# Performance work log

Measured on AMD Instinct MI355X. Metric: run time of the kernel, lower is better.

The kernel has to match this reference:

```python
import jax, jax.numpy as jnp
import numpy as np

N_NODES = 100000
N_EDGES = 1000000
N_GRAPHS = 4096
F_IN = 9
H = 64


def setup_inputs() -> dict:
    key = jax.random.key(0)
    ks = jax.random.split(key, 12)
    x = jax.random.normal(ks[0], (N_NODES, F_IN), dtype=jnp.float32)
    edge_index = jax.random.randint(ks[1], (2, N_EDGES), 0, N_NODES, dtype=jnp.int64)
    batch = jnp.sort(jax.random.randint(ks[2], (N_NODES,), 0, N_GRAPHS, dtype=jnp.int64))
    def lin(k, fan_in, fan_out):
        s = 1.0 / np.sqrt(fan_in)
        return jax.random.uniform(k, (fan_in, fan_out), jnp.float32, -s, s)
    return {
        "x": x, "edge_index": edge_index, "batch": batch,
        "W1": lin(ks[3], F_IN, H), "b1": jnp.zeros((H,), jnp.float32),
        "W2": lin(ks[4], H, H),    "b2": jnp.zeros((H,), jnp.float32),
        "W3": lin(ks[5], H, H),    "b3": jnp.zeros((H,), jnp.float32),
        "W4": lin(ks[6], H, H),    "b4": jnp.zeros((H,), jnp.float32),
        "Wout": lin(ks[7], H, 1),  "bout": jnp.zeros((1,), jnp.float32),
    }


def reference(x, edge_index, batch, W1, b1, W2, b2, W3, b3, W4, b4, Wout, bout):
    N = x.shape[0]
    loops = jnp.arange(N, dtype=edge_index.dtype)
    src = jnp.concatenate([edge_index[0], loops])  # messages flow src -> dst (PyG source_to_target)
    dst = jnp.concatenate([edge_index[1], loops])
    # symmetric GCN normalization with self-loops: deg includes self-loop
    deg = jax.ops.segment_sum(jnp.ones_like(dst, dtype=x.dtype), dst, num_segments=N)
    dis = jax.lax.rsqrt(jnp.maximum(deg, 1.0))  # deg >= 1 thanks to self-loops
    norm = dis[src] * dis[dst]                  # [E+N]

    def gcn_conv(h, W, b):
        h = h @ W                                # transform first (PyG order)
        msgs = h[src] * norm[:, None]            # [E+N, H]
        return jax.ops.segment_sum(msgs, dst, num_segments=N) + b

    h = jax.nn.relu(gcn_conv(x, W1, b1))
    h = jax.nn.relu(gcn_conv(h, W2, b2))
    h = jax.nn.relu(gcn_conv(h, W3, b3))
    h = jax.nn.relu(gcn_conv(h, W4, b4))

    # global mean pool over graphs
    sums = jax.ops.segment_sum(h, batch, num_segments=N_GRAPHS)      # [G, H]
    counts = jax.ops.segment_sum(jnp.ones((N,), h.dtype), batch, num_segments=N_GRAPHS)
    pooled = sums / jnp.maximum(counts, 1.0)[:, None]
    return pooled @ Wout + bout                  # [G, 1]
```

## Files before the change

### kernel.cpp

```cpp
#include <hip/hip_runtime.h>
#include <hip/hip_fp16.h>


static inline size_t align256(size_t x){ return (x + 255) & ~size_t(255); }

#define CHUNK 4096
#define SCAP  3072

struct __align__(8)  h4v { __half2 a, b; };
struct __align__(16) h8v { __half2 a, b, c, d; };

typedef _Float16 f16x8 __attribute__((ext_vector_type(8)));
typedef float    f32x4 __attribute__((ext_vector_type(4)));

__global__ __launch_bounds__(256) void k_sortchunk(
    const int* __restrict__ src, const int* __restrict__ dst,
    int* __restrict__ binned, int* __restrict__ hoffC, int E){
  __shared__ int hcnt[1024];
  __shared__ int simg[CHUNK];
  int c = blockIdx.x, t = threadIdx.x;
  int e0 = c*CHUNK;
  int cnt = E - e0; if (cnt > CHUNK) cnt = CHUNK;

  for (int i = t; i < 1024; i += 256) hcnt[i] = 0;
  __syncthreads();

  int bA[8], rA[8], vA[8], bB[8], rB[8], vB[8];
  #pragma unroll
  for (int j = 0; j < 8; j++){
    int i = t + j*256;
    if (i < cnt){
      int d = dst[e0+i];
      int s = src[e0+i];
      int b = d >> 7;
      bA[j] = b;
      rA[j] = atomicAdd(&hcnt[b], 1);
      vA[j] = (s << 7) | (d & 127);
    } else bA[j] = -1;
  }
  #pragma unroll
  for (int j = 0; j < 8; j++){
    int i = t + 2048 + j*256;
    if (i < cnt){
      int d = dst[e0+i];
      int s = src[e0+i];
      int b = d >> 7;
      bB[j] = b;
      rB[j] = atomicAdd(&hcnt[b], 1);
      vB[j] = (s << 7) | (d & 127);
    } else bB[j] = -1;
  }
  __syncthreads();

  int own[4];
  #pragma unroll
  for (int j = 0; j < 4; j++) own[j] = hcnt[t + j*256];
  for (int off = 1; off < 1024; off <<= 1){
    int nv[4];
    #pragma unroll
    for (int j = 0; j < 4; j++){
      int i = t + j*256;
      nv[j] = hcnt[i] + ((i >= off) ? hcnt[i-off] : 0);
    }
    __syncthreads();
    #pragma unroll
    for (int j = 0; j < 4; j++) hcnt[t + j*256] = nv[j];
    __syncthreads();
  }
  #pragma unroll
  for (int j = 0; j < 4; j++) hcnt[t + j*256] -= own[j];
  __syncthreads();

  for (int i = t; i < 783; i += 256) hoffC[c*783 + i] = hcnt[i];

  #pragma unroll
  for (int j = 0; j < 8; j++)
    if (bA[j] >= 0) simg[hcnt[bA[j]] + rA[j]] = vA[j];
  #pragma unroll
  for (int j = 0; j < 8; j++)
    if (bB[j] >= 0) simg[hcnt[bB[j]] + rB[j]] = vB[j];
  __syncthreads();

  for (int i = t; i < cnt; i += 256) binned[e0 + i] = simg[i];
}

__global__ __launch_bounds__(256) void k_bktsum(
    const int* __restrict__ hoffC, int* __restrict__ btot,
    float* __restrict__ gsum, int NC, int NBK, int G){
  __shared__ int s[256];
  int b = blockIdx.x, t = threadIdx.x;
  int gid = b*256 + t;
  if (gid < G) gsum[gid] = 0.f;
  int tot = 0;
  for (int c = t; c < NC; c += 256)
    tot += hoffC[c*783 + b + 1] - hoffC[c*783 + b];
  s[t] = tot; __syncthreads();
  for (int off = 128; off > 0; off >>= 1){
    if (t < off) s[t] += s[t+off];
    __syncthreads();
  }
  if (t == 0) btot[b] = s[0];
}

__global__ __launch_bounds__(256) void k_gather2(
    const int* __restrict__ binned, const int* __restrict__ hoffC,
    const int* __restrict__ btot, const float* __restrict__ x,
    int* __restrict__ row_ptr, float* __restrict__ dis,
    float* __restrict__ xs, int* __restrict__ csr, int N, int NC, int E){
  __shared__ int lcur[128];
  __shared__ int lscan[128];
  __shared__ float ldis[128];
  __shared__ int stage[SCAP];
  __shared__ int scount;
  __shared__ int sbb;
  int b = blockIdx.x, t = threadIdx.x;
  int n0 = b << 7;
  int nn = N - n0; if (nn > 128) nn = 128;

  int psum = 0;
  for (int i = t; i < b; i += 256) psum += btot[i];
  stage[t] = psum; __syncthreads();
  for (int off = 128; off > 0; off >>= 1){
    if (t < off) stage[t] += stage[t+off];
    __syncthreads();
  }
  if (t == 0) sbb = stage[0];
  if (t == 0 && b == 0) row_ptr[N] = E;
  if (t < 128) lcur[t] = 0;
  if (t == 0) scount = 0;
  __syncthreads();

  for (int c = t; c < NC; c += 256){
    int o0 = hoffC[c*783 + b];
    int o1 = hoffC[c*783 + b + 1];
    int len = o1 - o0;
    if (len > 0){
      int base = atomicAdd(&scount, len);
      int sbase = c*CHUNK;
      for (int k = 0; k < len; k++){
        int v = binned[sbase + o0 + k];
        atomicAdd(&lcur[v & 127], 1);
        int pos = base + k;
        if (pos < SCAP) stage[pos] = v;
      }
    }
  }
  __syncthreads();
  int degv = (t < 128) ? lcur[t] : 0;
  if (t < 128) lscan[t] = degv;
  __syncthreads();
  for (int off = 1; off < 128; off <<= 1){
    int add = (t < 128 && t >= off) ? lscan[t-off] : 0;
    __syncthreads();
    if (t < 128) lscan[t] += add;
    __syncthreads();
  }
  int bb = sbb;
  if (t < nn){
    int row = bb + lscan[t] - degv;
    row_ptr[n0 + t] = row;
    float dv = rsqrtf((float)(degv + 1));
    dis[n0 + t] = dv;
    ldis[t] = dv;
    lcur[t] = row;
  }
  __syncthreads();
  for (int i = t; i < nn*9; i += 256)
    xs[(size_t)n0*9 + i] = x[(size_t)n0*9 + i] * ldis[i/9];
  int sc = scount;
  if (sc <= SCAP){
    for (int i = t; i < sc; i += 256){
      int v = stage[i];
      int pos = atomicAdd(&lcur[v & 127], 1);
      csr[pos] = v >> 7;
    }
  } else {
    for (int c = t; c < NC; c += 256){
      int o0 = hoffC[c*783 + b];
      int o1 = hoffC[c*783 + b + 1];
      int sbase = c*CHUNK;
      for (int k = o0; k < o1; k++){
        int v = binned[sbase + k];
        int pos = atomicAdd(&lcur[v & 127], 1);
        csr[pos] = v >> 7;
      }
    }
  }
}

__global__ void k_agg9(const float* __restrict__ xs, const float* __restrict__ dis,
                       const int* __restrict__ row_ptr, const int* __restrict__ csr,
                       float* __restrict__ xagg, int N){
  int tid = blockIdx.x*blockDim.x + threadIdx.x;
  if (tid >= N*9) return;
  int n = tid/9, f = tid - n*9;
  float dn = dis[n];
  int s0 = row_ptr[n], s1 = row_ptr[n+1];
  float a0 = xs[tid];
  float a1 = 0.f, a2 = 0.f, a3 = 0.f;
  int j = s0;
  for (; j + 3 < s1; j += 4){
    int e0 = csr[j], e1 = csr[j+1], e2 = csr[j+2], e3 = csr[j+3];
    a0 += xs[e0*9+f];
    a1 += xs[e1*9+f];
    a2 += xs[e2*9+f];
    a3 += xs[e3*9+f];
  }
  for (; j < s1; j++) a0 += xs[csr[j]*9+f];
  xagg[tid] = ((a0+a1)+(a2+a3))*dn;
}

__device__ __forceinline__ void mfma_epilogue(
    const _Float16* hlw, const f16x8 (&wf)[4][2],
    __half* __restrict__ mo, int wid, int nwaves, int N, int lane){
  int lm = lane & 15, lk = lane >> 4;
  f16x8 hb0 = *(const f16x8*)(hlw + lm*72 + lk*8);
  f16x8 hb1 = *(const f16x8*)(hlw + lm*72 + 32 + lk*8);
  int node = wid + lm*nwaves;
  bool ok = (node < N);
  __half* row = mo + (size_t)node*64;
  #pragma unroll
  for (int ft = 0; ft < 4; ft++){
    f32x4 acc = {0.f, 0.f, 0.f, 0.f};
    acc = __builtin_amdgcn_mfma_f32_16x16x32_f16(wf[ft][0], hb0, acc, 0, 0, 0);
    acc = __builtin_amdgcn_mfma_f32_16x16x32_f16(wf[ft][1], hb1, acc, 0, 0, 0);
    if (ok){
      h4v o;
      o.a = __floats2half2_rn(acc[0], acc[1]);
      o.b = __floats2half2_rn(acc[2], acc[3]);
      *(h4v*)(row + ft*16 + lk*4) = o;
    }
  }
}

#define LOAD_WFRAGS(Wn)                                                    \
  f16x8 wf[4][2];                                                          \
  { int lm_ = lane & 15, lk_ = lane >> 4;                                  \
    _Pragma("unroll") for (int ft = 0; ft < 4; ft++)                       \
    _Pragma("unroll") for (int kb = 0; kb < 2; kb++)                       \
    _Pragma("unroll") for (int j = 0; j < 8; j++)                          \
      wf[ft][kb][j] = (_Float16)Wn[(kb*32 + lk_*8 + j)*64 + ft*16 + lm_]; }

__global__ __launch_bounds__(256) void k_lin1_fused(
    const float* __restrict__ xagg, const float* __restrict__ W1,
    const float* __restrict__ b1, const float* __restrict__ dis,
    const float* __restrict__ W2, __half* __restrict__ mo, int N, int nwaves){
  __shared__ float W1l[576];
  __shared__ float b1l[64];
  __shared__ _Float16 hl[4][16*72];
  int t = threadIdx.x;
  for (int i = t; i < 576; i += 256) W1l[i] = W1[i];
  if (t < 64) b1l[t] = b1[t];
  __syncthreads();
  int lane = t & 63, w = t >> 6;
  int wid = (blockIdx.x*blockDim.x + t) >> 6;
  LOAD_WFRAGS(W2)
  _Float16* hlw = hl[w];
  for (int i = 0; i < 16; i++){
    int n = wid + i*nwaves;
    _Float16 hv = (_Float16)0.f;
    if (n < N){
      float acc = b1l[lane];
      #pragma unroll
      for (int k = 0; k < 9; k++) acc = fmaf(xagg[n*9+k], W1l[k*64+lane], acc);
      hv = (_Float16)(fmaxf(acc, 0.f) * dis[n]);
    }
    hlw[i*72 + lane] = hv;
  }
  mfma_epilogue(hlw, wf, mo, wid, nwaves, N, lane);
}

#define ACC8(g_)  do{ float2 t_;                                   \
  t_ = __half22float2((g_).a); acc0 += t_.x; acc1 += t_.y;         \
  t_ = __half22float2((g_).b); acc2 += t_.x; acc3 += t_.y;         \
  t_ = __half22float2((g_).c); acc4 += t_.x; acc5 += t_.y;         \
  t_ = __half22float2((g_).d); acc6 += t_.x; acc7 += t_.y; }while(0)

#define RED3(v)  do{ v += __shfl_xor(v, 8,64);                     \
                     v += __shfl_xor(v,16,64);                     \
                     v += __shfl_xor(v,32,64); }while(0)

#define AGG_ISSUE(n_, rp0_, rp1_, rn0_, rn1_, e0_, e1_, g0_, g1_, sf_, dn_) \
  do{                                                                      \
    int nn_ = (n_) + 2*nwaves;                                             \
    rn0_ = 0; rn1_ = 0;                                                    \
    if (nn_ < N){ rn0_ = row_ptr[nn_]; rn1_ = row_ptr[nn_+1]; }            \
    e0_ = -1; e1_ = -1;                                                    \
    if ((n_) < N){                                                         \
      sf_ = m[(size_t)(n_)*8 + q2];                                        \
      dn_ = dis[n_];                                                       \
      int j0_ = (rp0_) + sub, j1_ = (rp0_) + 8 + sub;                      \
      if (j0_ < (rp1_)) e0_ = csr[j0_];                                    \
      if (j1_ < (rp1_)) e1_ = csr[j1_];                                    \
      if (e0_ >= 0) g0_ = m[(size_t)e0_*8 + q2];                           \
      if (e1_ >= 0) g1_ = m[(size_t)e1_*8 + q2];                           \
    }                                                                      \
  }while(0)

#define AGG_ACCRED(n_, rp0_, rp1_, e0_, e1_, g0_, g1_, sf_, dn_)           \
      float acc0=0.f,acc1=0.f,acc2=0.f,acc3=0.f;                           \
      float acc4=0.f,acc5=0.f,acc6=0.f,acc7=0.f;                           \
      if (e0_ >= 0) ACC8(g0_);                                             \
      if (e1_ >= 0) ACC8(g1_);                                             \
      for (int j_ = (rp0_) + 16 + sub; j_ < (rp1_); j_ += 8){              \
        h8v gx_ = m[(size_t)csr[j_]*8 + q2]; ACC8(gx_);                    \
      }                                                                    \
      RED3(acc0); RED3(acc1); RED3(acc2); RED3(acc3);                      \
      RED3(acc4); RED3(acc5); RED3(acc6); RED3(acc7);                      \
      float2 s01=__half22float2((sf_).a), s23=__half22float2((sf_).b);     \
      float2 s45=__half22float2((sf_).c), s67=__half22float2((sf_).d);     \
      float r0 = fmaxf(fmaf(acc0 + s01.x, dn_, bb0.x), 0.f);               \
      float r1 = fmaxf(fmaf(acc1 + s01.y, dn_, bb0.y), 0.f);               \
      float r2 = fmaxf(fmaf(acc2 + s23.x, dn_, bb0.z), 0.f);               \
      float r3 = fmaxf(fmaf(acc3 + s23.y, dn_, bb0.w), 0.f);               \
      float r4 = fmaxf(fmaf(acc4 + s45.x, dn_, bb1.x), 0.f);               \
      float r5 = fmaxf(fmaf(acc5 + s45.y, dn_, bb1.y), 0.f);               \
      float r6 = fmaxf(fmaf(acc6 + s67.x, dn_, bb1.z), 0.f);               \
      float r7 = fmaxf(fmaf(acc7 + s67.y, dn_, bb1.w), 0.f);

#define AGG_REDUCE(n_, rp0_, rp1_, e0_, e1_, g0_, g1_, sf_, dn_, i_)       \
  do{                                                                      \
    if ((n_) < N){                                                         \
      AGG_ACCRED(n_, rp0_, rp1_, e0_, e1_, g0_, g1_, sf_, dn_)             \
      if (sub == 0){                                                       \
        h8v hv_;                                                           \
        hv_.a = __floats2half2_rn(r0*(dn_), r1*(dn_));                     \
        hv_.b = __floats2half2_rn(r2*(dn_), r3*(dn_));                     \
        hv_.c = __floats2half2_rn(r4*(dn_), r5*(dn_));                     \
        hv_.d = __floats2half2_rn(r6*(dn_), r7*(dn_));                     \
        *(h8v*)(hlw + (i_)*72 + q2*8) = hv_;                               \
      }                                                                    \
    } else if (sub == 0){                                                  \
      h8v z_; z_.a = __floats2half2_rn(0.f, 0.f);                          \
      z_.b = z_.a; z_.c = z_.a; z_.d = z_.a;                               \
      *(h8v*)(hlw + (i_)*72 + q2*8) = z_;                                  \
    }                                                                      \
  }while(0)

__global__ __launch_bounds__(256) void k_agg_fused(
    const h8v* __restrict__ m, const float* __restrict__ dis,
    const float* __restrict__ b, const float* __restrict__ Wn,
    const int* __restrict__ row_ptr, const int* __restrict__ csr,
    __half* __restrict__ mo, int N, int nwaves){
  __shared__ _Float16 hl[4][16*72];
  int t = threadIdx.x;
  int lane = t & 63, w = t >> 6;
  int sub = lane >> 3, q2 = lane & 7;
  int wid = (blockIdx.x*blockDim.x + t) >> 6;
  _Float16* hlw = hl[w];
  const float4* b4 = (const float4*)b;
  float4 bb0 = b4[q2*2], bb1 = b4[q2*2+1];

  int nA = wid,          rA0 = 0, rA1 = 0;
  int nB = wid + nwaves, rB0 = 0, rB1 = 0;
  if (nA < N){ rA0 = row_ptr[nA]; rA1 = row_ptr[nA+1]; }
  if (nB < N){ rB0 = row_ptr[nB]; rB1 = row_ptr[nB+1]; }
  int eA0, eA1, eB0, eB1, rnA0, rnA1, rnB0, rnB1;
  h8v gA0, gA1, sfA, gB0, gB1, sfB;
  float dnA = 0.f, dnB = 0.f;
  AGG_ISSUE(nA, rA0, rA1, rnA0, rnA1, eA0, eA1, gA0, gA1, sfA, dnA);
  for (int p = 0; p < 8; p++){
    AGG_ISSUE(nB, rB0, rB1, rnB0, rnB1, eB0, eB1, gB0, gB1, sfB, dnB);
    AGG_REDUCE(nA, rA0, rA1, eA0, eA1, gA0, gA1, sfA, dnA, 2*p);
    nA += 2*nwaves; rA0 = rnA0; rA1 = rnA1;
    if (p < 7)
      AGG_ISSUE(nA, rA0, rA1, rnA0, rnA1, eA0, eA1, gA0, gA1, sfA, dnA);
    AGG_REDUCE(nB, rB0, rB1, eB0, eB1, gB0, gB1, sfB, dnB, 2*p+1);
    nB += 2*nwaves; rB0 = rnB0; rB1 = rnB1;
  }
  LOAD_WFRAGS(Wn)
  mfma_epilogue(hlw, wf, mo, wid, nwaves, N, lane);
}

__global__ __launch_bounds__(256) void k_agg64_out(
    const h8v* __restrict__ m, const float* __restrict__ dis,
    const float* __restrict__ b, const float* __restrict__ Wout,
    const int* __restrict__ batch,
    const int* __restrict__ row_ptr, const int* __restrict__ csr,
    float* gsum, int N, int nwaves){
  int lane = threadIdx.x & 63;
  int sub = lane >> 3, q2 = lane & 7;
  int n = (blockIdx.x*blockDim.x + threadIdx.x) >> 6;
  if (n >= N) return;
  const float4* b4 = (const float4*)b;
  const float4* wo4 = (const float4*)Wout;
  float4 bb0 = b4[q2*2], bb1 = b4[q2*2+1];
  float4 w0 = wo4[q2*2], w1 = wo4[q2*2+1];

  int rp0 = row_ptr[n], rp1 = row_ptr[n+1];
  int n1 = n + nwaves;
  int rq0 = 0, rq1 = 0;
  if (n1 < N){ rq0 = row_ptr[n1]; rq1 = row_ptr[n1+1]; }
  int e0 = -1, e1 = -1;
  { int j0 = rp0 + sub, j1 = rp0 + 8 + sub;
    if (j0 < rp1) e0 = csr[j0];
    if (j1 < rp1) e1 = csr[j1]; }
  while (true){
    h8v g0, g1, sf;
    if (e0 >= 0) g0 = m[(size_t)e0*8 + q2];
    if (e1 >= 0) g1 = m[(size_t)e1*8 + q2];
    sf = m[(size_t)n*8 + q2];
    float dn = dis[n];
    int bg = batch[n];
    int n2 = n1 + nwaves;
    int rr0 = 0, rr1 = 0;
    if (n2 < N){ rr0 = row_ptr[n2]; rr1 = row_ptr[n2+1]; }
    int f0 = -1, f1 = -1;
    if (n1 < N){
      int j0 = rq0 + sub, j1 = rq0 + 8 + sub;
      if (j0 < rq1) f0 = csr[j0];
      if (j1 < rq1) f1 = csr[j1];
    }
    AGG_ACCRED(n, rp0, rp1, e0, e1, g0, g1, sf, dn)
    float p = r0*w0.x + r1*w0.y + r2*w0.z + r3*w0.w
            + r4*w1.x + r5*w1.y + r6*w1.z + r7*w1.w;
    p += __shfl_xor(p,1,64); p += __shfl_xor(p,2,64); p += __shfl_xor(p,4,64);
    if (lane == 0) atomicAdd(&gsum[bg], p);
    if (n1 >= N) break;
    n = n1; rp0 = rq0; rp1 = rq1;
    n1 = n2; rq0 = rr0; rq1 = rr1;
    e0 = f0; e1 = f1;
  }
}

__global__ void k_final(const float* __restrict__ gsum, const int* __restrict__ batch,
                        const float* __restrict__ bout, float* __restrict__ out,
                        int G, int N){
  int g = blockIdx.x*blockDim.x + threadIdx.x;
  if (g >= G) return;
  int lo = 0, hi = N;
  while (lo < hi){ int mid = (lo+hi)>>1; if (batch[mid] <  g) lo = mid+1; else hi = mid; }
  int lb = lo;
  lo = 0; hi = N;
  while (lo < hi){ int mid = (lo+hi)>>1; if (batch[mid] <= g) lo = mid+1; else hi = mid; }
  int c = lo - lb;
  out[g] = gsum[g]/(float)(c > 0 ? c : 1) + bout[0];
}

extern "C" void kernel_launch(void* const* d_in, const int* in_sizes, int n_in,
                              void* d_out, int out_size, void* d_ws, size_t ws_size,
                              hipStream_t stream){
  const float* x    = (const float*)d_in[0];
  const int*   ei   = (const int*)d_in[1];
  const int*   batch= (const int*)d_in[2];
  const float* W1 = (const float*)d_in[3];  const float* b1 = (const float*)d_in[4];
  const float* W2 = (const float*)d_in[5];  const float* b2 = (const float*)d_in[6];
  const float* W3 = (const float*)d_in[7];  const float* b3 = (const float*)d_in[8];
  const float* W4 = (const float*)d_in[9];  const float* b4 = (const float*)d_in[10];
  const float* Wout = (const float*)d_in[11]; const float* bout = (const float*)d_in[12];
  float* out = (float*)d_out;

  const int N = in_sizes[0]/9;
  const int E = in_sizes[1]/2;
  const int G = out_size;
  const int* src = ei;
  const int* dst = ei + E;

  char* ws = (char*)d_ws;
  size_t off = 0;
  auto alloc = [&](size_t bytes){ void* p = ws + off; off = align256(off + bytes); return p; };
  int*   row_ptr  = (int*)  alloc((size_t)(N+1)*4);
  int*   csr      = (int*)  alloc((size_t)E*4);
  float* dis      = (float*)alloc((size_t)N*4);
  const int NBK = (N + 127)/128;
  const int NC  = (E + CHUNK-1)/CHUNK;
  int*   hoffC    = (int*)  alloc((size_t)NC*783*4);
  int*   btot     = (int*)  alloc((size_t)NBK*4);
  float* gsum     = (float*)alloc((size_t)G*4);
  __half* mA      = (__half*)alloc((size_t)N*64*2);
  __half* mB      = (__half*)alloc((size_t)N*64*2);
  int*   binned   = (int*)mA;
  float* xs       = (float*)mB;
  float* xagg     = xs + (size_t)N*9;

  const int AGG_BLOCKS = 2048;
  const int AGG_WAVES  = AGG_BLOCKS*4;

  k_sortchunk<<<NC, 256, 0, stream>>>(src, dst, binned, hoffC, E);
  k_bktsum   <<<NBK, 256, 0, stream>>>(hoffC, btot, gsum, NC, NBK, G);
  k_gather2  <<<NBK, 256, 0, stream>>>(binned, hoffC, btot, x,
                                       row_ptr, dis, xs, csr, N, NC, E);

  k_agg9  <<<(N*9+255)/256, 256, 0, stream>>>(xs, dis, row_ptr, csr, xagg, N);
  k_lin1_fused<<<AGG_BLOCKS, 256, 0, stream>>>(xagg, W1, b1, dis, W2, mA, N, AGG_WAVES);

  k_agg_fused<<<AGG_BLOCKS, 256, 0, stream>>>((const h8v*)mA, dis, b2, W3,
                                              row_ptr, csr, mB, N, AGG_WAVES);
  k_agg_fused<<<AGG_BLOCKS, 256, 0, stream>>>((const h8v*)mB, dis, b3, W4,
                                              row_ptr, csr, mA, N, AGG_WAVES);
  k_agg64_out<<<AGG_BLOCKS, 256, 0, stream>>>((const h8v*)mA, dis, b4, Wout, batch,
                                              row_ptr, csr, gsum, N, AGG_WAVES);

  k_final<<<(G+255)/256, 256, 0, stream>>>(gsum, batch, bout, out, G, N);
}
```

Measured before the change: 299.7 us.

## Pad input features to 12 floats and aggregate layer-1 per node with float4

Scaled input features are stored padded to 12 floats per node so the first aggregation can run one thread per node with three float4 gathers per neighbor, instead of nine scalar threads per node each re-reading the CSR indices. The final aggregation kernel also drops its cross-iteration software pipelining of row pointers and neighbor indices in favor of a simpler loop that loads edges and features inline. The padding adds 33% more storage and traffic for xs and xagg, and the one-thread-per-node layout gives less parallelism and uncoalesced per-thread loads.

```diff
diff --git a/kernel.cpp b/kernel.cpp
--- a/kernel.cpp
+++ b/kernel.cpp
@@ -165,8 +165,11 @@
     lcur[t] = row;
   }
   __syncthreads();
-  for (int i = t; i < nn*9; i += 256)
-    xs[(size_t)n0*9 + i] = x[(size_t)n0*9 + i] * ldis[i/9];
+  for (int i = t; i < nn*12; i += 256){
+    int node = i/12, f = i - node*12;
+    xs[(size_t)(n0+node)*12 + f] =
+        (f < 9) ? x[(size_t)(n0+node)*9 + f] * ldis[node] : 0.f;
+  }
   int sc = scount;
   if (sc <= SCAP){
     for (int i = t; i < sc; i += 256){
@@ -188,26 +191,38 @@
   }
 }
 
-__global__ void k_agg9(const float* __restrict__ xs, const float* __restrict__ dis,
-                       const int* __restrict__ row_ptr, const int* __restrict__ csr,
-                       float* __restrict__ xagg, int N){
-  int tid = blockIdx.x*blockDim.x + threadIdx.x;
-  if (tid >= N*9) return;
-  int n = tid/9, f = tid - n*9;
+#define F4ADD(d_, s_) do{ d_.x += s_.x; d_.y += s_.y; d_.z += s_.z; d_.w += s_.w; }while(0)
+
+__global__ __launch_bounds__(256) void k_agg9(
+    const float4* __restrict__ xs4, const float* __restrict__ dis,
+    const int* __restrict__ row_ptr, const int* __restrict__ csr,
+    float4* __restrict__ xagg4, int N){
+  int n = blockIdx.x*blockDim.x + threadIdx.x;
+  if (n >= N) return;
   float dn = dis[n];
   int s0 = row_ptr[n], s1 = row_ptr[n+1];
-  float a0 = xs[tid];
-  float a1 = 0.f, a2 = 0.f, a3 = 0.f;
+  float4 a0 = xs4[(size_t)n*3], a1 = xs4[(size_t)n*3+1], a2 = xs4[(size_t)n*3+2];
+  float4 b0 = {0,0,0,0}, b1 = b0, b2 = b0;
   int j = s0;
-  for (; j + 3 < s1; j += 4){
-    int e0 = csr[j], e1 = csr[j+1], e2 = csr[j+2], e3 = csr[j+3];
-    a0 += xs[e0*9+f];
-    a1 += xs[e1*9+f];
-    a2 += xs[e2*9+f];
-    a3 += xs[e3*9+f];
-  }
-  for (; j < s1; j++) a0 += xs[csr[j]*9+f];
-  xagg[tid] = ((a0+a1)+(a2+a3))*dn;
+  for (; j + 1 < s1; j += 2){
+    int e0 = csr[j], e1 = csr[j+1];
+    float4 p0 = xs4[(size_t)e0*3], p1 = xs4[(size_t)e0*3+1], p2 = xs4[(size_t)e0*3+2];
+    float4 q0 = xs4[(size_t)e1*3], q1 = xs4[(size_t)e1*3+1], q2 = xs4[(size_t)e1*3+2];
+    F4ADD(a0,p0); F4ADD(a1,p1); F4ADD(a2,p2);
+    F4ADD(b0,q0); F4ADD(b1,q1); F4ADD(b2,q2);
+  }
+  if (j < s1){
+    int e0 = csr[j];
+    float4 p0 = xs4[(size_t)e0*3], p1 = xs4[(size_t)e0*3+1], p2 = xs4[(size_t)e0*3+2];
+    F4ADD(a0,p0); F4ADD(a1,p1); F4ADD(a2,p2);
+  }
+  F4ADD(a0,b0); F4ADD(a1,b1); F4ADD(a2,b2);
+  a0.x *= dn; a0.y *= dn; a0.z *= dn; a0.w *= dn;
+  a1.x *= dn; a1.y *= dn; a1.z *= dn; a1.w *= dn;
+  a2.x *= dn; a2.y *= dn; a2.z *= dn; a2.w *= dn;
+  xagg4[(size_t)n*3]   = a0;
+  xagg4[(size_t)n*3+1] = a1;
+  xagg4[(size_t)n*3+2] = a2;
 }
 
 __device__ __forceinline__ void mfma_epilogue(
@@ -262,7 +277,7 @@
     if (n < N){
       float acc = b1l[lane];
       #pragma unroll
-      for (int k = 0; k < 9; k++) acc = fmaf(xagg[n*9+k], W1l[k*64+lane], acc);
+      for (int k = 0; k < 9; k++) acc = fmaf(xagg[(size_t)n*12+k], W1l[k*64+lane], acc);
       hv = (_Float16)(fmaxf(acc, 0.f) * dis[n]);
     }
     hlw[i*72 + lane] = hv;
@@ -382,44 +397,44 @@
   int sub = lane >> 3, q2 = lane & 7;
   int n = (blockIdx.x*blockDim.x + threadIdx.x) >> 6;
   if (n >= N) return;
+  int rp0 = row_ptr[n], rp1 = row_ptr[n+1];
   const float4* b4 = (const float4*)b;
   const float4* wo4 = (const float4*)Wout;
-  float4 bb0 = b4[q2*2], bb1 = b4[q2*2+1];
-  float4 w0 = wo4[q2*2], w1 = wo4[q2*2+1];
-
-  int rp0 = row_ptr[n], rp1 = row_ptr[n+1];
-  int n1 = n + nwaves;
-  int rq0 = 0, rq1 = 0;
-  if (n1 < N){ rq0 = row_ptr[n1]; rq1 = row_ptr[n1+1]; }
-  int e0 = -1, e1 = -1;
-  { int j0 = rp0 + sub, j1 = rp0 + 8 + sub;
-    if (j0 < rp1) e0 = csr[j0];
-    if (j1 < rp1) e1 = csr[j1]; }
   while (true){
-    h8v g0, g1, sf;
-    if (e0 >= 0) g0 = m[(size_t)e0*8 + q2];
-    if (e1 >= 0) g1 = m[(size_t)e1*8 + q2];
-    sf = m[(size_t)n*8 + q2];
+    int nn = n + nwaves;
+    int np0 = 0, np1 = 0;
+    if (nn < N){ np0 = row_ptr[nn]; np1 = row_ptr[nn+1]; }
+    h8v sf = m[(size_t)n*8 + q2];
     float dn = dis[n];
     int bg = batch[n];
-    int n2 = n1 + nwaves;
-    int rr0 = 0, rr1 = 0;
-    if (n2 < N){ rr0 = row_ptr[n2]; rr1 = row_ptr[n2+1]; }
-    int f0 = -1, f1 = -1;
-    if (n1 < N){
-      int j0 = rq0 + sub, j1 = rq0 + 8 + sub;
-      if (j0 < rq1) f0 = csr[j0];
-      if (j1 < rq1) f1 = csr[j1];
-    }
-    AGG_ACCRED(n, rp0, rp1, e0, e1, g0, g1, sf, dn)
+    float acc0=0.f,acc1=0.f,acc2=0.f,acc3=0.f,acc4=0.f,acc5=0.f,acc6=0.f,acc7=0.f;
+    int s1 = rp1;
+    int j0 = rp0 + sub, j1 = rp0 + 8 + sub;
+    if (j0 < s1){ h8v a = m[(size_t)csr[j0]*8 + q2]; ACC8(a); }
+    if (j1 < s1){ h8v a = m[(size_t)csr[j1]*8 + q2]; ACC8(a); }
+    for (int j = rp0 + 16 + sub; j < s1; j += 8){
+      h8v a = m[(size_t)csr[j]*8 + q2]; ACC8(a);
+    }
+    RED3(acc0); RED3(acc1); RED3(acc2); RED3(acc3);
+    RED3(acc4); RED3(acc5); RED3(acc6); RED3(acc7);
+    float2 s01 = __half22float2(sf.a), s23 = __half22float2(sf.b);
+    float2 s45 = __half22float2(sf.c), s67 = __half22float2(sf.d);
+    float4 bb0 = b4[q2*2], bb1 = b4[q2*2+1];
+    float4 w0 = wo4[q2*2], w1 = wo4[q2*2+1];
+    float r0 = fmaxf(fmaf(acc0 + s01.x, dn, bb0.x), 0.f);
+    float r1 = fmaxf(fmaf(acc1 + s01.y, dn, bb0.y), 0.f);
+    float r2 = fmaxf(fmaf(acc2 + s23.x, dn, bb0.z), 0.f);
+    float r3 = fmaxf(fmaf(acc3 + s23.y, dn, bb0.w), 0.f);
+    float r4 = fmaxf(fmaf(acc4 + s45.x, dn, bb1.x), 0.f);
+    float r5 = fmaxf(fmaf(acc5 + s45.y, dn, bb1.y), 0.f);
+    float r6 = fmaxf(fmaf(acc6 + s67.x, dn, bb1.z), 0.f);
+    float r7 = fmaxf(fmaf(acc7 + s67.y, dn, bb1.w), 0.f);
     float p = r0*w0.x + r1*w0.y + r2*w0.z + r3*w0.w
             + r4*w1.x + r5*w1.y + r6*w1.z + r7*w1.w;
     p += __shfl_xor(p,1,64); p += __shfl_xor(p,2,64); p += __shfl_xor(p,4,64);
     if (lane == 0) atomicAdd(&gsum[bg], p);
-    if (n1 >= N) break;
-    n = n1; rp0 = rq0; rp1 = rq1;
-    n1 = n2; rq0 = rr0; rq1 = rr1;
-    e0 = f0; e1 = f1;
+    if (nn >= N) break;
+    n = nn; rp0 = np0; rp1 = np1;
   }
 }
 
@@ -471,7 +486,7 @@
   __half* mB      = (__half*)alloc((size_t)N*64*2);
   int*   binned   = (int*)mA;
   float* xs       = (float*)mB;
-  float* xagg     = xs + (size_t)N*9;
+  float* xagg     = xs + (size_t)N*12;
 
   const int AGG_BLOCKS = 2048;
   const int AGG_WAVES  = AGG_BLOCKS*4;
@@ -481,7 +496,8 @@
   k_gather2  <<<NBK, 256, 0, stream>>>(binned, hoffC, btot, x,
                                        row_ptr, dis, xs, csr, N, NC, E);
 
-  k_agg9  <<<(N*9+255)/256, 256, 0, stream>>>(xs, dis, row_ptr, csr, xagg, N);
+  k_agg9  <<<(N+255)/256, 256, 0, stream>>>((const float4*)xs, dis, row_ptr, csr,
+                                            (float4*)xagg, N);
   k_lin1_fused<<<AGG_BLOCKS, 256, 0, stream>>>(xagg, W1, b1, dis, W2, mA, N, AGG_WAVES);
 
   k_agg_fused<<<AGG_BLOCKS, 256, 0, stream>>>((const h8v*)mA, dis, b2, W3,
```

Result: no change. 299.2 us, median of 2 (-0.2%).
